# Kernel tuning notes

Hardware: AMD Instinct MI355X
Metric: run time of the kernel (lower is better)

The kernel has to match this reference:

```python
import jax, jax.numpy as jnp
import numpy as np
from jax import lax

SCALES = [0.5, 1, 2]


def resize_bilinear_ac(x, oh, ow):
    """F.interpolate(mode='bilinear', align_corners=True) for NCHW x."""
    B, C, H, W = x.shape
    def coords(n_in, n_out):
        c = jnp.linspace(0.0, n_in - 1.0, n_out).astype(x.dtype)
        i0 = jnp.clip(jnp.floor(c).astype(jnp.int32), 0, n_in - 1)
        i1 = jnp.minimum(i0 + 1, n_in - 1)
        return i0, i1, c - i0.astype(x.dtype)
    y0, y1, wy = coords(H, oh)
    x0, x1, wx = coords(W, ow)
    top = x[:, :, y0, :] * (1 - wy)[:, None] + x[:, :, y1, :] * wy[:, None]
    return top[:, :, :, x0] * (1 - wx) + top[:, :, :, x1] * wx


def interpolate4d(t, oh, ow):
    """Geometry.interpolate4d: bilinear resize of both spatial pairs of [b,h1,w1,h2,w2]."""
    b, h1, w1, h2, w2 = t.shape
    t = t.reshape(b, h1, w1, h2 * w2).transpose(0, 3, 1, 2)
    t = resize_bilinear_ac(t, oh, ow)            # [b, h2*w2, oh, ow]
    t = t.reshape(b, h2, w2, oh * ow).transpose(0, 3, 1, 2)
    t = resize_bilinear_ac(t, oh, ow)            # [b, oh*ow, oh, ow]
    return t.reshape(b, oh, ow, oh, ow)


def conv2d_same(x, w):
    return lax.conv_general_dilated(x, w, (1, 1), [(1, 1), (1, 1)],
                                    dimension_numbers=('NCHW', 'OIHW', 'NCHW'))


def conv3d_same(x, w, p):
    return lax.conv_general_dilated(x, w, (1, 1, 1), [(p, p)] * 3,
                                    dimension_numbers=('NCDHW', 'OIDHW', 'NCDHW'))


def fast4d(corr, kernel, bias=None):
    """4D conv (stride 1, same zero-padding) via per-slice 3D convs, mirroring chm.fast4d.
    corr: [b, ci, sh, sw, th, tw]; kernel: [co, ci, k, k, k, k]."""
    b, ci, sh, sw, th, tw = corr.shape
    co, k = kernel.shape[0], kernel.shape[2]
    p = k // 2
    x = corr.transpose(0, 2, 1, 3, 4, 5).reshape(b * sh, ci, sw, th, tw)
    out = jnp.zeros((b, co, sh, sw, th, tw), corr.dtype)
    for pidx in range(k):
        ic = conv3d_same(x, kernel[:, :, pidx], p)
        ic = ic.reshape(b, sh, co, sw, th, tw).transpose(0, 2, 1, 3, 4, 5)
        a0, a1 = max(p - pidx, 0), min(sh, sh + p - pidx)
        s0, s1 = max(pidx - p, 0), min(sh, sh + pidx - p)
        out = out.at[:, :, a0:a1].add(ic[:, :, s0:s1])
    if bias is not None:
        out = out + bias.reshape(1, co, 1, 1, 1, 1)
    return out


def chm6d(corr, kernel):
    """6D conv with kernel (K,K,kk,kk,kk,kk), same zero-padding, no bias (chm.fast6d).
    corr: [b, 1, S, S, h, w, h, w]; kernel: [1, 1, K, K, kk, kk, kk, kk]."""
    b, _, S, _, h, w, _, _ = corr.shape
    K, kk = kernel.shape[2], kernel.shape[4]
    pk = K // 2
    x = corr.transpose(0, 2, 3, 1, 4, 5, 6, 7).reshape(b * S * S, 1, h, w, h, w)
    ker = kernel.reshape(1, K * K, kk, kk, kk, kk).swapaxes(0, 1)  # [K*K, 1, kk...]
    y = fast4d(x, ker).reshape(b, S, S, K * K, h, w, h, w)
    yp = jnp.pad(y, ((0, 0), (pk, pk), (pk, pk), (0, 0), (0, 0), (0, 0), (0, 0), (0, 0)))
    out = jnp.zeros((b, S, S, h, w, h, w), corr.dtype)
    for ki in range(K):
        for kj in range(K):
            out = out + yp[:, ki:ki + S, kj:kj + S, ki * K + kj]
    return out[:, None]


def mutual_nn_filter(cm):
    smax = jnp.max(cm, axis=2, keepdims=True)
    tmax = jnp.max(cm, axis=1, keepdims=True)
    smax = jnp.where(smax == 0, 1e-30, smax)
    tmax = jnp.where(tmax == 0, 1e-30, tmax)
    return cm * ((cm / smax) * (cm / tmax))


def build_correlation6d(src_feat, trg_feat, conv_ws):
    bsz, _, side, _ = src_feat.shape
    sfs, tfs = [], []
    for scale, w in zip(SCALES, conv_ws):
        s = int(np.floor(scale * side))
        sfs.append(conv2d_same(resize_bilinear_ac(src_feat, s, s), w))
        tfs.append(conv2d_same(resize_bilinear_ac(trg_feat, s, s), w))
    corr6d = []
    for sf in sfs:
        ch, ss = sf.shape[1], sf.shape[-1]
        sv = sf.reshape(bsz, ch, ss * ss).transpose(0, 2, 1)   # [b, ss^2, ch]
        sn = jnp.linalg.norm(sv, axis=2, keepdims=True)
        for tf in tfs:
            ts = tf.shape[-1]
            tv = tf.reshape(bsz, ch, ts * ts)                  # [b, ch, ts^2]
            tn = jnp.linalg.norm(tv, axis=1, keepdims=True)
            c = jnp.einsum('bsc,bct->bst', sv, tv) / (sn * tn)
            corr6d.append(interpolate4d(c.reshape(bsz, ss, ss, ts, ts), side, side))
    corr = jnp.stack(corr6d).reshape(3, 3, bsz, side, side, side, side)
    corr = corr.transpose(2, 0, 1, 3, 4, 5, 6)                 # [b, 3, 3, s, s, s, s]
    return jnp.maximum(corr, 0.0)


def chm_forward(src_feat, trg_feat, w0, w1, w2, k6, k4, b4):
    bsz, _, side, _ = src_feat.shape
    corr = build_correlation6d(src_feat, trg_feat, (w0, w1, w2))[:, None]
    corr = jax.nn.sigmoid(chm6d(corr, k6))                     # [b,1,3,3,h,w,h,w]
    h = w = side
    corr = corr.reshape(bsz, -1, h, w, h, w).max(axis=1)       # max over 9 scale pairs
    corr = interpolate4d(corr, 2 * h, 2 * w)[:, None]          # [b,1,2h,2w,2h,2w]
    corr = jax.nn.softplus(fast4d(corr, k4, b4)[:, 0])
    n = corr.shape[-1] ** 2
    return mutual_nn_filter(corr.reshape(bsz, n, n))


def setup_inputs() -> dict:
    key = jax.random.key(0)
    ks = jax.random.split(key, 8)
    b, fd, side = 4, 1024, 16
    w_std = 0.02  # ~kaiming for 3x3 conv with fan_in 1024*9
    return {
        'src_feat': jax.random.normal(ks[0], (b, fd, side, side), jnp.float32),
        'trg_feat': jax.random.normal(ks[1], (b, fd, side, side), jnp.float32),
        'conv_w0': jax.random.normal(ks[2], (fd // 4, fd, 3, 3), jnp.float32) * w_std,
        'conv_w1': jax.random.normal(ks[3], (fd // 4, fd, 3, 3), jnp.float32) * w_std,
        'conv_w2': jax.random.normal(ks[4], (fd // 4, fd, 3, 3), jnp.float32) * w_std,
        'chm6d_w': jax.random.normal(ks[5], (1, 1, 3, 3, 5, 5, 5, 5), jnp.float32) * 0.05,
        'chm4d_w': jax.random.normal(ks[6], (1, 1, 5, 5, 5, 5), jnp.float32) * 0.05,
        'chm4d_b': jnp.zeros((1,), jnp.float32),
    }


def reference(src_feat, trg_feat, conv_w0, conv_w1, conv_w2, chm6d_w, chm4d_w, chm4d_b):
    return chm_forward(src_feat, trg_feat, conv_w0, conv_w1, conv_w2, chm6d_w, chm4d_w, chm4d_b)
```

## Files before the change

### kernel.cpp

```cpp
#include <hip/hip_runtime.h>
#include <cstdint>
#include <cstddef>


#define DEVFN __device__ __forceinline__

typedef __attribute__((ext_vector_type(8))) short short8v;
typedef __attribute__((ext_vector_type(4))) float f32x4;
typedef unsigned int u32;

DEVFN void gl_lds16(const void* g, void* l){
  __builtin_amdgcn_global_load_lds(
      (const __attribute__((address_space(1))) u32*)g,
      (__attribute__((address_space(3))) u32*)l, 16, 0, 0);
}

constexpr size_t OFF_WB    = 0;
constexpr size_t OFF_P8    = 3538944;
constexpr size_t OFF_P16   = 3948544;
constexpr size_t OFF_P32   = 5275648;
constexpr size_t OFF_SF8   = 10010624;
constexpr size_t OFF_TF8   = 10076160;
constexpr size_t OFF_SF16  = 10141696;
constexpr size_t OFF_TF16  = 10403840;
constexpr size_t OFF_SF32  = 10665984;
constexpr size_t OFF_TF32  = 11714560;
constexpr size_t OFF_INVS  = 12763136;
constexpr size_t OFF_INVT  = 12768512;
constexpr size_t OFF_TMAX  = 12777984;
constexpr size_t OFF_CORR6 = 12782080;
constexpr size_t OFF_CMAXP = OFF_CORR6 + 2359296 + 128;
constexpr size_t OFF_WA    = OFF_CMAXP + 131072;
constexpr size_t OFF_PARTK = OFF_WA + 96128;
constexpr size_t OFF_SMAXP = OFF_PARTK + 2752512;
constexpr size_t OFF_WA4   = OFF_SMAXP + 16384;
constexpr size_t OFF_FB3   = OFF_WA4 + 12800;
constexpr size_t WS_FLOATS = OFF_FB3 + 1376256;

__device__ constexpr size_t PAIR_OFF[9] = {
  OFF_WB + 0,       OFF_WB + 16384,   OFF_WB + 81920,
  OFF_WB + 344064,  OFF_WB + 409600,  OFF_WB + 671744,
  OFF_WB + 1720320, OFF_WB + 1982464, OFF_WB + 3031040 };
constexpr size_t OFF_CL    = 0;
constexpr size_t OFF_MAXED = 9437184;
constexpr size_t OFF_INT32 = 262144;

__device__ constexpr int SSARR[3] = {8, 16, 32};
__device__ constexpr int PAIR_START[9] = {0,4,20,84,100,164,420,484,740};

DEVFN unsigned short f2bf(float f){
  unsigned int u = __float_as_uint(f);
  return (unsigned short)((u + 0x7fffu + ((u >> 16) & 1u)) >> 16);
}
DEVFN float bf2f(unsigned short u){
  return __uint_as_float(((unsigned int)u) << 16);
}

__global__ __launch_bounds__(256) void k_wpack(const float* __restrict__ w0,
                                               const float* __restrict__ w1,
                                               const float* __restrict__ w2,
                                               float* __restrict__ wsf){
  int bx = blockIdx.x;
  int scale = bx >> 8, cg = (bx >> 4) & 15, ig = bx & 15;
  const float* w = (scale==0) ? w0 : (scale==1 ? w1 : w2);
  const int t = threadIdx.x;
  __shared__ float sW[16*580];
  const float* src = w + (size_t)cg*16*9216 + (size_t)ig*576;
  for (int i=t; i<9216; i+=256){
    int co = i/576, r = i%576;
    sW[co*580 + r] = src[(size_t)co*9216 + r];
  }
  __syncthreads();
  unsigned short* ob = (unsigned short*)(wsf + OFF_WB) + (size_t)scale*2359296;
  for (int f=t; f<1152; f+=256){
    int tap = f/128, rem = f%128, kcl = rem>>6, l = rem&63;
    int kc = ig*2 + kcl;
    int co = l & 15;
    int ciL = kcl*32 + ((l>>4)&3)*8;
    unsigned short* o = ob + ((size_t)tap*32768 + (size_t)kc*1024 + (size_t)cg*64 + l)*8;
    #pragma unroll
    for (int i=0;i<8;i++)
      o[i] = f2bf(sW[co*580 + (ciL+i)*9 + tap]);
  }
}

__global__ void k_wa(const float* __restrict__ k6, float* __restrict__ wsf){
  int gid = blockIdx.x*256 + threadIdx.x;
  if (gid >= 24000) return;
  int tap = gid / 192, rem = gid % 192;
  int kc = rem / 64, l = rem % 64;
  int d = tap % 5, ac = tap / 5, a = ac / 5, c = ac % 5;
  int so = l & 15, k8 = (l >> 4) * 8;
  unsigned short* o = (unsigned short*)(wsf + OFF_WA) + (size_t)gid*8;
  #pragma unroll
  for (int i=0;i<8;i++){
    int kg = kc*32 + k8 + i;
    int e = kg >> 4, pr = kg & 15;
    float v = 0.f;
    if (so < 9 && pr < 9 && e < 5){
      int pi = pr/3, pj = pr%3, sio = so/3, sjo = so%3;
      int ki = pi - sio + 1, kj = pj - sjo + 1;
      if (ki>=0 && ki<=2 && kj>=0 && kj<=2)
        v = k6[(((((ki*3+kj)*5 + a)*5 + c)*5 + d)*5) + e];
    }
    o[i] = f2bf(v);
  }
}

__global__ void k_wa4(const float* __restrict__ k4, float* __restrict__ wsf){
  int gid = blockIdx.x*256 + threadIdx.x;
  if (gid >= 3200) return;
  int d = gid / 640, rem = gid % 640;
  int kc = rem / 64, l = rem % 64;
  int so = l & 15, soy = so >> 2, sox = so & 3;
  int e = kc >> 1;
  int pyw = 4*(kc & 1) + (l >> 4);
  unsigned short* o = (unsigned short*)(wsf + OFF_WA4) + (size_t)gid*8;
  #pragma unroll
  for (int i=0;i<8;i++){
    int a = pyw - soy, c = i - sox;
    float v = 0.f;
    if (a>=0 && a<=4 && c>=0 && c<=4)
      v = k4[((a*5 + c)*5 + d)*5 + e];
    o[i] = f2bf(v);
  }
}

__global__ __launch_bounds__(256) void k_inpack(const float* __restrict__ src,
                                                const float* __restrict__ trg,
                                                float* __restrict__ wsf){
  int bt = blockIdx.x >> 6, cg = blockIdx.x & 63;
  int chbase = cg*16;
  int t = threadIdx.x;
  __shared__ float sIn[16][257];
  const float* gin = ((bt>=4)? trg : src) + ((size_t)(bt&3)*1024 + chbase)*256;
  #pragma unroll
  for (int i=0;i<16;i++){
    int idx = t + i*256; int ch = idx>>8, pos = idx&255;
    sIn[ch][pos] = gin[(size_t)ch*256 + pos];
  }
  __syncthreads();
  int ch = t & 15, pw = t >> 4;
  #pragma unroll 1
  for (int s=0; s<3; s++){
    int S = SSARR[s], Sp = S+2, Sp2 = Sp*Sp;
    size_t poff = (s==0)?OFF_P8 : (s==1)?OFF_P16 : OFF_P32;
    unsigned short* o = (unsigned short*)(wsf + poff) + (size_t)bt*Sp2*1024 + chbase + ch;
    float rs = 15.f/(float)(S-1);
    for (int i = pw; i < Sp2; i += 16){
      int py = i / Sp, px = i % Sp;
      float v = 0.f;
      if (py>0 && py<Sp-1 && px>0 && px<Sp-1){
        float cy = (float)(py-1)*rs, cx = (float)(px-1)*rs;
        int y0 = (int)cy; if (y0>15) y0=15; int y1 = (y0+1<16)?y0+1:15; float fy = cy-(float)y0;
        int x0 = (int)cx; if (x0>15) x0=15; int x1 = (x0+1<16)?x0+1:15; float fx = cx-(float)x0;
        v = (1.f-fy)*((1.f-fx)*sIn[ch][y0*16+x0] + fx*sIn[ch][y0*16+x1])
          +       fy*((1.f-fx)*sIn[ch][y1*16+x0] + fx*sIn[ch][y1*16+x1]);
      }
      o[(size_t)i*1024] = f2bf(v);
    }
  }
}

__global__ __launch_bounds__(256) void k_conv_mfma(float* __restrict__ wsf){
  int bxid = blockIdx.x;
  int scale, bt, cot, post, ks, S, lgS;
  if (bxid < 512){
    int xcd = bxid & 7, j2 = bxid >> 3;
    int g = (j2 >> 5)*8 + xcd;
    int j = j2 & 31;
    scale = 2; S = 32; lgS = 5;
    bt = g >> 1; cot = g & 1; post = j >> 1; ks = j & 1;
  } else {
    int r = bxid - 512;
    ks = r & 1; int bx = 256 + (r >> 1);
    if (bx < 320){ int q=bx-256; scale=1; S=16; lgS=4; bt=q>>3; cot=(q>>2)&1; post=q&3; }
    else         { int q=bx-320; scale=0; S=8;  lgS=3; bt=q>>1; cot=q&1; post=0; }
  }
  const int Sp = S+2, N = S*S;
  const unsigned short* WbS = (const unsigned short*)(wsf + OFF_WB) + (size_t)scale*2359296;
  size_t poff = scale==0?OFF_P8: scale==1?OFF_P16:OFF_P32;
  const unsigned short* Pb = (const unsigned short*)(wsf + poff) + (size_t)bt*Sp*Sp*1024;
  size_t obase = (scale==2) ? (bt>=4?OFF_TF32:OFF_SF32)
               : (scale==1) ? (bt>=4?OFF_TF16:OFF_SF16)
                            : (bt>=4?OFF_TF8 :OFF_SF8);
  if (ks) obase += OFF_PARTK - OFF_SF8;
  float* outp = wsf + obase + (size_t)(bt&3)*256*N;

  const int t = threadIdx.x, l = t&63, w = t>>6, wm = w&1, wn = w>>1;
  const int nc_base = cot*8;
  const int pos0 = post*64;
  const int it0 = ks*72, it1 = it0 + 72;

  __shared__ __align__(16) unsigned short Ab[2][8192];
  __shared__ __align__(16) unsigned short Bb[2][4096];

  f32x4 acc[4][2];
  #pragma unroll
  for (int i=0;i<4;i++)
    #pragma unroll
    for (int j=0;j<2;j++) acc[i][j] = (f32x4){0.f,0.f,0.f,0.f};

  auto STAGE = [&](int buf, int it){
    int tap = it>>4, kq = it&15;
    int dy = tap/3, dx = tap - dy*3;
    #pragma unroll
    for (int j=0;j<4;++j){
      int c = w + j*4;
      int kc = c>>3, nc = c&7;
      const unsigned short* src =
        WbS + ((((size_t)tap*32 + kq*2 + kc)*16 + nc_base + nc)*64 + l)*8;
      gl_lds16(src, &Ab[buf][c*512]);
    }
    #pragma unroll
    for (int j=0;j<2;++j){
      int c = w + j*4;
      int kc = c>>2, np = c&3;
      int pos = pos0 + np*16 + (l&15);
      int y = pos>>lgS, x = pos&(S-1);
      int row = (y+dy)*Sp + (x+dx);
      int ci = kq*64 + kc*32 + ((l>>4)<<3);
      gl_lds16(Pb + (size_t)row*1024 + ci, &Bb[buf][c*512]);
    }
  };

  STAGE(0, it0);
  __syncthreads();
  int buf = 0;
  #pragma unroll 1
  for (int it=it0; it<it1; ++it){
    if (it+1 < it1) STAGE(buf^1, it+1);
    #pragma unroll
    for (int kc=0; kc<2; ++kc){
      short8v a0 = *(const short8v*)&Ab[buf][((kc*8 + wm*4 + 0)*64 + l)*8];
      short8v a1 = *(const short8v*)&Ab[buf][((kc*8 + wm*4 + 1)*64 + l)*8];
      short8v a2 = *(const short8v*)&Ab[buf][((kc*8 + wm*4 + 2)*64 + l)*8];
      short8v a3 = *(const short8v*)&Ab[buf][((kc*8 + wm*4 + 3)*64 + l)*8];
      short8v b0 = *(const short8v*)&Bb[buf][((kc*4 + wn*2 + 0)*64 + l)*8];
      short8v b1 = *(const short8v*)&Bb[buf][((kc*4 + wn*2 + 1)*64 + l)*8];
      acc[0][0] = __builtin_amdgcn_mfma_f32_16x16x32_bf16(a0, b0, acc[0][0], 0,0,0);
      acc[1][0] = __builtin_amdgcn_mfma_f32_16x16x32_bf16(a1, b0, acc[1][0], 0,0,0);
      acc[2][0] = __builtin_amdgcn_mfma_f32_16x16x32_bf16(a2, b0, acc[2][0], 0,0,0);
      acc[3][0] = __builtin_amdgcn_mfma_f32_16x16x32_bf16(a3, b0, acc[3][0], 0,0,0);
      acc[0][1] = __builtin_amdgcn_mfma_f32_16x16x32_bf16(a0, b1, acc[0][1], 0,0,0);
      acc[1][1] = __builtin_amdgcn_mfma_f32_16x16x32_bf16(a1, b1, acc[1][1], 0,0,0);
      acc[2][1] = __builtin_amdgcn_mfma_f32_16x16x32_bf16(a2, b1, acc[2][1], 0,0,0);
      acc[3][1] = __builtin_amdgcn_mfma_f32_16x16x32_bf16(a3, b1, acc[3][1], 0,0,0);
    }
    __syncthreads();
    buf ^= 1;
  }

  const int r0 = (l>>4)*4, cl = l&15;
  float* ob = outp + (size_t)(cot*128 + wm*64)*N + pos0 + wn*32 + cl;
  #pragma unroll
  for (int mf=0; mf<4; ++mf)
    #pragma unroll
    for (int nf=0; nf<2; ++nf){
      float* op = ob + (size_t)(mf*16 + r0)*N + nf*16;
      #pragma unroll
      for (int i=0;i<4;++i) op[(size_t)i*N] = acc[mf][nf][i];
    }
}

__global__ __launch_bounds__(256) void k_fbpack(float* __restrict__ ws){
  int bx = blockIdx.x;
  int tsr = bx/84, r = bx%84;
  int s, b, chunk;
  if (r < 4)       { s=0; b=r;        chunk=0; }
  else if (r < 20) { s=1; int q=r-4;  b=q>>2; chunk=q&3; }
  else             { s=2; int q=r-20; b=q>>4; chunk=q&15; }
  int P = SSARR[s]*SSARR[s];
  size_t fbase = (s==0)? (tsr?OFF_TF8 :OFF_SF8)
               : (s==1)? (tsr?OFF_TF16:OFF_SF16)
                       : (tsr?OFF_TF32:OFF_SF32);
  const float* src = ws + fbase + (size_t)b*256*P;
  const float* prt = ws + OFF_PARTK + (fbase - OFF_SF8) + (size_t)b*256*P;
  int pos0 = chunk*64;
  const int t = threadIdx.x;
  __shared__ float tile[64][260];
  for (int i=0;i<64;i++){
    int idx = t + i*256; int ch = idx>>6, pl = idx&63;
    size_t o = (size_t)ch*P + pos0 + pl;
    tile[pl][ch] = src[o] + prt[o];
  }
  __syncthreads();
  int rowbase = tsr*5376 + (s==0?0: s==1?256:1280) + b*P + pos0;
  unsigned short* FB = (unsigned short*)(ws + OFF_FB3);
  for (int i=0;i<64;i++){
    int idx = t + i*256; int pl = idx>>8, ch = idx&255;
    FB[(size_t)(rowbase+pl)*256 + ch] = f2bf(tile[pl][ch]);
  }
}

__global__ void k_invnorm(float* __restrict__ ws){
  int gid = blockIdx.x*256 + threadIdx.x;
  int row = gid >> 4, sub = gid & 15;
  const unsigned short* fb = (const unsigned short*)(ws + OFF_FB3)
                           + (size_t)row*256 + sub*16;
  float s = 0.f;
  #pragma unroll
  for (int i=0;i<2;i++){
    short8v v = *(const short8v*)(fb + i*8);
    #pragma unroll
    for (int j=0;j<8;j++){
      float f = bf2f(((unsigned short*)&v)[j]);
      s = fmaf(f, f, s);
    }
  }
  #pragma unroll
  for (int m=1; m<16; m<<=1) s += __shfl_xor(s, m);
  if (sub == 0){
    int tsr = row/5376, r = row%5376;
    ws[(tsr ? OFF_INVT : OFF_INVS) + r] = 1.f/sqrtf(s);
  }
}

__global__ __launch_bounds__(256) void k_corr(float* __restrict__ ws){
  int bx = blockIdx.x;
  int p = (bx>=4)+(bx>=20)+(bx>=84)+(bx>=100)+(bx>=164)+(bx>=420)+(bx>=484)+(bx>=740);
  int si = p/3, ti = p%3;
  int M = SSARR[si]*SSARR[si], N = SSARR[ti]*SSARR[ti];
  int ntN = N >> 6;
  int rem = bx - PAIR_START[p];
  int b = rem & 3; rem >>= 2;
  int nt = rem % ntN, mt = rem / ntN;
  int m0 = mt*64, n0 = nt*64;
  const unsigned short* FB = (const unsigned short*)(ws + OFF_FB3);
  const unsigned short* Ap = FB + (size_t)((si==0?0: si==1?256:1280) + b*M + m0)*256;
  const unsigned short* Bp = FB + (size_t)(5376 + (ti==0?0: ti==1?256:1280) + b*N + n0)*256;
  const int t = threadIdx.x, l = t&63, w = t>>6, wm = w&1, wn = w>>1;
  const int mrow = wm*32 + (l&15), ncol = wn*32 + (l&15);
  f32x4 acc[2][2];
  #pragma unroll
  for (int i=0;i<2;i++)
    #pragma unroll
    for (int j=0;j<2;j++) acc[i][j] = (f32x4){0.f,0.f,0.f,0.f};
  #pragma unroll
  for (int ksp=0; ksp<8; ++ksp){
    const int ko = ksp*32 + ((l>>4)&3)*8;
    short8v a0 = *(const short8v*)(Ap + (size_t) mrow     *256 + ko);
    short8v a1 = *(const short8v*)(Ap + (size_t)(mrow+16) *256 + ko);
    short8v b0 = *(const short8v*)(Bp + (size_t) ncol     *256 + ko);
    short8v b1 = *(const short8v*)(Bp + (size_t)(ncol+16) *256 + ko);
    acc[0][0] = __builtin_amdgcn_mfma_f32_16x16x32_bf16(a0, b0, acc[0][0], 0,0,0);
    acc[1][0] = __builtin_amdgcn_mfma_f32_16x16x32_bf16(a1, b0, acc[1][0], 0,0,0);
    acc[0][1] = __builtin_amdgcn_mfma_f32_16x16x32_bf16(a0, b1, acc[0][1], 0,0,0);
    acc[1][1] = __builtin_amdgcn_mfma_f32_16x16x32_bf16(a1, b1, acc[1][1], 0,0,0);
  }
  const float* iS = ws + OFF_INVS + (si==0?0: si==1?256:1280) + (size_t)b*M;
  const float* iT = ws + OFF_INVT + (ti==0?0: ti==1?256:1280) + (size_t)b*N;
  float* C = ws + PAIR_OFF[p] + (size_t)b*M*N;
  const int r0 = (l>>4)*4, cl = l&15;
  #pragma unroll
  for (int mf=0; mf<2; ++mf)
    #pragma unroll
    for (int nf=0; nf<2; ++nf)
      #pragma unroll
      for (int i=0;i<4;++i){
        int m = m0 + wm*32 + mf*16 + r0 + i;
        int n = n0 + wn*32 + nf*16 + cl;
        C[(size_t)m*N + n] = acc[mf][nf][i]*iS[m]*iT[n];
      }
}

DEVFN void cw_coord(int i, int n, int OH, int& i0, int& i1, float& f){
  float c = (float)(i*(n-1))/(float)(OH-1);
  int a = (int)c; if (a > n-1) a = n-1;
  i0 = a; i1 = (a+1 < n) ? a+1 : n-1; f = c - (float)a;
}

__global__ __launch_bounds__(256) void k_interp_pairs(float* __restrict__ ws){
  int bx = blockIdx.x;
  int p = bx >> 10;
  int bl = bx & 1023;
  int b = bl >> 8, oy = (bl >> 4) & 15, ox = bl & 15;
  int si = p/3, ti = p%3;
  int h1 = SSARR[si], t1 = SSARR[ti], t12 = t1*t1;
  int y0,y1,x0,x1; float fy,fx;
  cw_coord(oy,h1,16,y0,y1,fy); cw_coord(ox,h1,16,x0,x1,fx);
  const float* in = ws + PAIR_OFF[p] + (size_t)b*h1*h1*t12;
  __shared__ float sPl[4][1024];
  const int t = threadIdx.x;
  {
    const float* pl0 = in + (size_t)(y0*h1+x0)*t12;
    const float* pl1 = in + (size_t)(y0*h1+x1)*t12;
    const float* pl2 = in + (size_t)(y1*h1+x0)*t12;
    const float* pl3 = in + (size_t)(y1*h1+x1)*t12;
    for (int i=t; i<t12; i+=256){
      sPl[0][i] = pl0[i]; sPl[1][i] = pl1[i];
      sPl[2][i] = pl2[i]; sPl[3][i] = pl3[i];
    }
  }
  __syncthreads();
  int px = t & 15, py = t >> 4;
  int u0,u1,v0,v1; float fu,fv;
  cw_coord(py,t1,16,u0,u1,fu); cw_coord(px,t1,16,v0,v1,fv);
  float wY[2]={1.f-fy,fy}, wX[2]={1.f-fx,fx};
  float wU[2]={1.f-fu,fu}, wV[2]={1.f-fv,fv};
  int us[2]={u0,u1}, vs[2]={v0,v1};
  float s = 0.f;
  #pragma unroll
  for (int qa=0; qa<2; qa++)
    #pragma unroll
    for (int qc=0; qc<2; qc++){
      float wyx = wY[qa]*wX[qc];
      const float* base = sPl[qa*2+qc];
      #pragma unroll
      for (int qu=0; qu<2; qu++)
        #pragma unroll
        for (int qv=0; qv<2; qv++)
          s += wyx*wU[qu]*wV[qv]*base[us[qu]*t1 + vs[qv]];
    }
  ws[OFF_CORR6 + ((size_t)b*9 + p)*65536 + ((size_t)(oy*16+ox)<<8) + t] = fmaxf(s, 0.f);
}

__global__ __launch_bounds__(256) void k_cl(float* __restrict__ ws){
  int bx = blockIdx.x;
  int b = bx >> 8, yx = bx & 255;
  const int t = threadIdx.x;
  __shared__ __align__(16) unsigned short tile[10080];
  for (int i=t; i<1260; i+=256)
    *reinterpret_cast<f32x4*>((float*)&tile[i*8]) = (f32x4){0.f,0.f,0.f,0.f};
  __syncthreads();
  const float* c6 = ws + OFF_CORR6 + ((size_t)b*9 << 16) + ((size_t)yx << 8);
  const int qy = t >> 4, qx = t & 15;
  const int wo = ((2+qy)*21 + 2+qx)*24;
  #pragma unroll
  for (int pr=0; pr<9; ++pr)
    tile[wo + pr] = f2bf(c6[((size_t)pr << 16) + t]);
  __syncthreads();
  unsigned short* o = (unsigned short*)(ws + OFF_CL) + (size_t)bx*10080;
  for (int i=t; i<1260; i+=256)
    *reinterpret_cast<f32x4*>((float*)&o[i*8]) =
      *reinterpret_cast<const f32x4*>((const float*)&tile[i*8]);
}

__global__ __launch_bounds__(256) void k_chm6d(float* __restrict__ ws){
  int id = (blockIdx.x & 7)*128 + (blockIdx.x >> 3);
  const int b = id >> 8, sy = (id >> 4) & 15, sx = id & 15;
  const int t = threadIdx.x, l = t & 63, w = t >> 6;
  const int x = l & 15, h = (l >> 4) & 1, e2 = (l >> 4) >> 1;
  const unsigned short* CLu = (const unsigned short*)(ws + OFF_CL);
  const unsigned short* WAu = (const unsigned short*)(ws + OFF_WA);
  __shared__ __align__(16) unsigned short tile[2][10080];

  f32x4 acc[4];
  #pragma unroll
  for (int i=0;i<4;i++) acc[i] = (f32x4){0.f,0.f,0.f,0.f};

  auto STAGE = [&](int buf, int YX){
    const unsigned short* src = CLu + (size_t)(b*256 + YX)*10080;
    #pragma unroll
    for (int j=0;j<5;++j){
      int ch = t + j*256;
      if (ch < 1260) gl_lds16(src + (size_t)ch*8, &tile[buf][ch*8]);
    }
  };

  const int xb0 = (x + e2)*24 + 8*h;

  int i0 = 0;
  for (; i0 < 25; ++i0){
    int Y = sy + i0/5 - 2, X = sx + i0%5 - 2;
    if (Y>=0 && Y<=15 && X>=0 && X<=15) break;
  }
  {
    int Y = sy + i0/5 - 2, X = sx + i0%5 - 2;
    STAGE(0, Y*16 + X);
  }
  __syncthreads();
  int buf = 0, i = i0;
  #pragma unroll 1
  while (i < 25){
    int nx = i + 1;
    for (; nx < 25; ++nx){
      int Y = sy + nx/5 - 2, X = sx + nx%5 - 2;
      if (Y>=0 && Y<=15 && X>=0 && X<=15) break;
    }
    if (nx < 25){
      int Y = sy + nx/5 - 2, X = sx + nx%5 - 2;
      STAGE(buf^1, Y*16 + X);
    }
    {
      const unsigned short* wa = WAu + (size_t)i*5*3*512;
      short8v afr[5][3];
      #pragma unroll
      for (int d=0; d<5; ++d)
        #pragma unroll
        for (int kc=0; kc<3; ++kc)
          afr[d][kc] = *(const short8v*)&wa[((d*3 + kc)*64 + l)*8];
      const unsigned short* tb = &tile[buf][0];
      #pragma unroll
      for (int rl=0; rl<8; ++rl){
        const int row = (w*4 + rl)*504;
        short8v bf0 = *(const short8v*)&tb[row + xb0];
        short8v bf1 = *(const short8v*)&tb[row + xb0 + 48];
        short8v bf2 = *(const short8v*)&tb[row + xb0 + 96];
        #pragma unroll
        for (int y=0; y<4; ++y){
          if (y <= rl && rl - y <= 4){
            const int d = rl - y;
            acc[y] = __builtin_amdgcn_mfma_f32_16x16x32_bf16(afr[d][0], bf0, acc[y], 0,0,0);
            acc[y] = __builtin_amdgcn_mfma_f32_16x16x32_bf16(afr[d][1], bf1, acc[y], 0,0,0);
            acc[y] = __builtin_amdgcn_mfma_f32_16x16x32_bf16(afr[d][2], bf2, acc[y], 0,0,0);
          }
        }
      }
    }
    __syncthreads();
    buf ^= 1; i = nx;
  }

  const int g = l >> 4;
  float* maxed = ws + OFF_MAXED + (size_t)b*65536 + (size_t)(sy*16+sx)*256;
  #pragma unroll
  for (int y=0; y<4; ++y){
    float lm;
    if (g < 2)      lm = fmaxf(fmaxf(acc[y][0], acc[y][1]), fmaxf(acc[y][2], acc[y][3]));
    else if (g==2)  lm = acc[y][0];
    else            lm = -1e30f;
    lm = fmaxf(lm, __shfl_xor(lm, 16));
    lm = fmaxf(lm, __shfl_xor(lm, 32));
    if (l < 16)
      maxed[(w*4 + y)*16 + x] = 1.f/(1.f + expf(-lm));
  }
}

__global__ void k_interp32(float* __restrict__ ws){
  int id = blockIdx.x*256 + threadIdx.x;
  int px = id & 31, py = (id>>5)&31, ox = (id>>10)&31, oy = (id>>15)&31, b = id>>20;
  int y0,y1,x0,x1,u0,u1,v0,v1; float fy,fx,fu,fv;
  cw_coord(oy,16,32,y0,y1,fy); cw_coord(ox,16,32,x0,x1,fx);
  cw_coord(py,16,32,u0,u1,fu); cw_coord(px,16,32,v0,v1,fv);
  const float* in = ws + OFF_MAXED + (size_t)b*65536;
  int ys[2]={y0,y1}, xs[2]={x0,x1}, us[2]={u0,u1}, vs[2]={v0,v1};
  float wy[2]={1.f-fy,fy}, wx[2]={1.f-fx,fx}, wu[2]={1.f-fu,fu}, wv[2]={1.f-fv,fv};
  float s = 0.f;
  #pragma unroll
  for (int ia=0; ia<2; ia++)
    #pragma unroll
    for (int ic=0; ic<2; ic++){
      float wyx = wy[ia]*wx[ic];
      const float* base = in + ((size_t)ys[ia]*16 + xs[ic])*256;
      #pragma unroll
      for (int id_=0; id_<2; id_++)
        #pragma unroll
        for (int ie=0; ie<2; ie++)
          s += wyx*wu[id_]*wv[ie]*base[(size_t)us[id_]*16 + vs[ie]];
    }
  ws[OFF_INT32 + id] = s;
}

__global__ __launch_bounds__(256) void k_fast4d(float* __restrict__ ws,
                                                const float* __restrict__ b4,
                                                float* __restrict__ out){
  int id = (blockIdx.x & 7)*128 + (blockIdx.x >> 3);
  const int b = id >> 8, rem = id & 255;
  const int syb = rem >> 5, sxb = (rem >> 2) & 7, yh = rem & 3;
  const int t = threadIdx.x, l = t & 63, w = t >> 6;
  __shared__ __align__(16) unsigned short T[27648];
  __shared__ float red[4][16];
  for (int i=t; i<3456; i+=256)
    *reinterpret_cast<f32x4*>((float*)&T[i*8]) = (f32x4){0.f,0.f,0.f,0.f};
  __syncthreads();
  const float* I = ws + OFF_INT32 + (size_t)b*1048576;
  #pragma unroll 4
  for (int j=0; j<48; ++j){
    int idx2 = j*256 + t;
    int xo = idx2 & 15, pl = (idx2>>4) & 63, ry = idx2 >> 10;
    int pya = syb*4 + (pl>>3) - 2;
    int pxa = sxb*4 + (pl&7) - 2;
    int rya = yh*8 + ry - 2;
    if (pya>=0 && pya<32 && pxa>=0 && pxa<32 && rya>=0 && rya<32){
      float2 v = *reinterpret_cast<const float2*>(
          I + (size_t)(pya*32+pxa)*1024 + rya*32 + xo*2);
      int base = (ry*36 + xo*2 + 2)*64 + pl;
      T[base]      = f2bf(v.x);
      T[base + 64] = f2bf(v.y);
    }
  }
  __syncthreads();
  const unsigned short* WA4 = (const unsigned short*)(ws + OFF_WA4);
  f32x4 acc[2][2];
  #pragma unroll
  for (int i=0;i<2;i++)
    #pragma unroll
    for (int j=0;j<2;j++) acc[i][j] = (f32x4){0.f,0.f,0.f,0.f};
  const unsigned short* Tl = T + (l&15)*64 + (l>>4)*8 + w*2*2304;
  #pragma unroll 1
  for (int d=0; d<5; ++d){
    short8v afr[10];
    #pragma unroll
    for (int kc=0; kc<10; ++kc)
      afr[kc] = *(const short8v*)&WA4[((size_t)(d*10 + kc)*64 + l)*8];
    #pragma unroll
    for (int y2=0; y2<2; ++y2){
      const unsigned short* Tr = Tl + (y2 + d)*2304;
      #pragma unroll
      for (int xg=0; xg<2; ++xg){
        const unsigned short* Tx = Tr + xg*1024;
        #pragma unroll
        for (int kc=0; kc<10; ++kc){
          short8v bf = *(const short8v*)&Tx[(kc>>1)*64 + (kc&1)*32];
          acc[y2][xg] = __builtin_amdgcn_mfma_f32_16x16x32_bf16(afr[kc], bf, acc[y2][xg], 0,0,0);
        }
      }
    }
  }
  const float bias = b4[0];
  float rm[4] = {-1e30f,-1e30f,-1e30f,-1e30f};
  #pragma unroll
  for (int y2=0; y2<2; ++y2)
    #pragma unroll
    for (int xg=0; xg<2; ++xg)
      #pragma unroll
      for (int i=0; i<4; ++i){
        int so = (l>>4)*4 + i;
        float xv = acc[y2][xg][i] + bias;
        float sp = fmaxf(xv,0.f) + log1pf(expf(-fabsf(xv)));
        int row = (syb*4 + (so>>2))*32 + sxb*4 + (so&3);
        int col = (yh*8 + w*2 + y2)*32 + xg*16 + (l&15);
        out[((size_t)b*1024 + row)*1024 + col] = sp;
        rm[i] = fmaxf(rm[i], sp);
      }
  #pragma unroll
  for (int m=1; m<16; m<<=1)
    #pragma unroll
    for (int i=0;i<4;++i) rm[i] = fmaxf(rm[i], __shfl_xor(rm[i], m));
  if ((l & 15) == 0){
    #pragma unroll
    for (int i=0;i<4;++i) red[w][(l>>4)*4 + i] = rm[i];
  }
  __syncthreads();
  if (t < 16){
    float m = fmaxf(fmaxf(red[0][t], red[1][t]), fmaxf(red[2][t], red[3][t]));
    int row = (syb*4 + (t>>2))*32 + sxb*4 + (t&3);
    ws[OFF_SMAXP + (size_t)yh*4096 + (size_t)b*1024 + row] = m;
  }
}

__global__ void k_colmax_p(const float* __restrict__ cm, float* __restrict__ ws){
  int b = blockIdx.x >> 7, rg = (blockIdx.x >> 2) & 31, cg = blockIdx.x & 3;
  int c = cg*256 + threadIdx.x;
  const float* base = cm + (size_t)b*1048576 + (size_t)rg*32768 + c;
  float m = -1e30f;
  #pragma unroll 4
  for (int r=0; r<32; r++) m = fmaxf(m, base[(size_t)r*1024]);
  ws[OFF_CMAXP + (size_t)(b*32+rg)*1024 + c] = m;
}

__global__ void k_colmax_r(float* __restrict__ ws){
  int id = blockIdx.x*256 + threadIdx.x;
  int b = id >> 10, c = id & 1023;
  float m = -1e30f;
  #pragma unroll
  for (int rg=0; rg<32; rg++)
    m = fmaxf(m, ws[OFF_CMAXP + (size_t)(b*32+rg)*1024 + c]);
  ws[OFF_TMAX + id] = m;
}

__global__ void k_mutual(float* __restrict__ cm, const float* __restrict__ ws){
  int id = blockIdx.x*256 + threadIdx.x;
  int b = id >> 20, r = (id>>10)&1023, c = id&1023;
  float v  = cm[id];
  size_t si = (size_t)(b<<10) + r;
  float sm = fmaxf(fmaxf(ws[OFF_SMAXP + si],        ws[OFF_SMAXP + 4096 + si]),
                   fmaxf(ws[OFF_SMAXP + 8192 + si], ws[OFF_SMAXP + 12288 + si]));
  float tm = ws[OFF_TMAX + (b<<10) + c];
  sm = (sm==0.f) ? 1e-30f : sm;
  tm = (tm==0.f) ? 1e-30f : tm;
  cm[id] = v * (v/sm) * (v/tm);
}

extern "C" void kernel_launch(void* const* d_in, const int* in_sizes, int n_in,
                              void* d_out, int out_size, void* d_ws, size_t ws_size,
                              hipStream_t stream){
  const float* src = (const float*)d_in[0];
  const float* trg = (const float*)d_in[1];
  const float* w0  = (const float*)d_in[2];
  const float* w1  = (const float*)d_in[3];
  const float* w2  = (const float*)d_in[4];
  const float* k6  = (const float*)d_in[5];
  const float* k4  = (const float*)d_in[6];
  const float* b4  = (const float*)d_in[7];
  float* ws  = (float*)d_ws;
  float* out = (float*)d_out;
  (void)in_sizes; (void)n_in; (void)out_size; (void)ws_size;

  k_wpack       <<<768,   256, 0, stream>>>(w0, w1, w2, ws);
  k_wa          <<<94,    256, 0, stream>>>(k6, ws);
  k_wa4         <<<13,    256, 0, stream>>>(k4, ws);
  k_inpack      <<<512,   256, 0, stream>>>(src, trg, ws);
  k_conv_mfma   <<<672,   256, 0, stream>>>(ws);
  k_fbpack      <<<168,   256, 0, stream>>>(ws);
  k_invnorm     <<<672,   256, 0, stream>>>(ws);
  k_corr        <<<1764,  256, 0, stream>>>(ws);
  k_interp_pairs<<<9216,  256, 0, stream>>>(ws);
  k_cl          <<<1024,  256, 0, stream>>>(ws);
  k_chm6d       <<<1024,  256, 0, stream>>>(ws);
  k_interp32    <<<16384, 256, 0, stream>>>(ws);
  k_fast4d      <<<1024,  256, 0, stream>>>(ws, b4, out);
  k_colmax_p    <<<512,   256, 0, stream>>>(out, ws);
  k_colmax_r    <<<16,    256, 0, stream>>>(ws);
  k_mutual      <<<16384, 256, 0, stream>>>(out, ws);
}
```

Before: 371.1 us.

## Widen conv MFMA tile to 128 positions and remap blocks across XCDs

The bf16 MFMA conv kernel is templated on the number of N-fragments, so scales 16 and 32 use a 128-position tile (4 N-fragments per wave) and scale 8 keeps 64. Each staged weight tile is therefore reused over twice as many positions, which halves weight reloads. The grid shrinks from 672 to 352 blocks and uses an XCD-interleaved block index. The cost is more accumulator registers, a larger B buffer in LDS (64 KB total), and fewer blocks to fill the CUs.

```diff
diff --git a/kernel.cpp b/kernel.cpp
--- a/kernel.cpp
+++ b/kernel.cpp
@@ -162,20 +162,93 @@
   }
 }
 
+template<int NF>
+DEVFN void conv_core(const unsigned short* __restrict__ WbS,
+                     const unsigned short* __restrict__ Pb,
+                     float* __restrict__ outp,
+                     int S, int lgS, int Sp, int N,
+                     int nc_base, int pos0, int it0, int it1, int t,
+                     unsigned short (&Ab)[2][8192], unsigned short (&Bb)[2][8192]){
+  const int l = t&63, w = t>>6, wm = w&1, wn = w>>1;
+  f32x4 acc[4][NF];
+  #pragma unroll
+  for (int i=0;i<4;i++)
+    #pragma unroll
+    for (int j=0;j<NF;j++) acc[i][j] = (f32x4){0.f,0.f,0.f,0.f};
+
+  auto STAGE = [&](int buf, int it){
+    int tap = it>>4, kq = it&15;
+    int dy = tap/3, dx = tap - dy*3;
+    #pragma unroll
+    for (int j=0;j<4;++j){
+      int c = w + j*4;
+      int kc = c>>3, nc = c&7;
+      const unsigned short* src =
+        WbS + ((((size_t)tap*32 + kq*2 + kc)*16 + nc_base + nc)*64 + l)*8;
+      gl_lds16(src, &Ab[buf][c*512]);
+    }
+    #pragma unroll
+    for (int j=0;j<NF;++j){
+      int c = w + j*4;
+      int kc = (NF==4)? (c>>3) : (c>>2);
+      int np = (NF==4)? (c&7)  : (c&3);
+      int pos = pos0 + np*16 + (l&15);
+      int y = pos>>lgS, x = pos&(S-1);
+      int row = (y+dy)*Sp + (x+dx);
+      int ci = kq*64 + kc*32 + ((l>>4)<<3);
+      gl_lds16(Pb + (size_t)row*1024 + ci, &Bb[buf][c*512]);
+    }
+  };
+
+  STAGE(0, it0);
+  __syncthreads();
+  int buf = 0;
+  #pragma unroll 1
+  for (int it=it0; it<it1; ++it){
+    if (it+1 < it1) STAGE(buf^1, it+1);
+    #pragma unroll
+    for (int kc=0; kc<2; ++kc){
+      short8v a[4], bv[NF];
+      #pragma unroll
+      for (int mf=0; mf<4; ++mf)
+        a[mf] = *(const short8v*)&Ab[buf][((kc*8 + wm*4 + mf)*64 + l)*8];
+      #pragma unroll
+      for (int nf=0; nf<NF; ++nf)
+        bv[nf] = *(const short8v*)&Bb[buf][((kc*(2*NF) + wn*NF + nf)*64 + l)*8];
+      #pragma unroll
+      for (int mf=0; mf<4; ++mf)
+        #pragma unroll
+        for (int nf=0; nf<NF; ++nf)
+          acc[mf][nf] = __builtin_amdgcn_mfma_f32_16x16x32_bf16(a[mf], bv[nf], acc[mf][nf], 0,0,0);
+    }
+    __syncthreads();
+    buf ^= 1;
+  }
+
+  const int r0 = (l>>4)*4, cl = l&15;
+  float* ob = outp + (size_t)(wm*64)*N + pos0 + wn*(NF*16) + cl;
+  #pragma unroll
+  for (int mf=0; mf<4; ++mf)
+    #pragma unroll
+    for (int nf=0; nf<NF; ++nf){
+      float* op = ob + (size_t)(mf*16 + r0)*N + nf*16;
+      #pragma unroll
+      for (int i=0;i<4;++i) op[(size_t)i*N] = acc[mf][nf][i];
+    }
+}
+
 __global__ __launch_bounds__(256) void k_conv_mfma(float* __restrict__ wsf){
-  int bxid = blockIdx.x;
-  int scale, bt, cot, post, ks, S, lgS;
-  if (bxid < 512){
-    int xcd = bxid & 7, j2 = bxid >> 3;
-    int g = (j2 >> 5)*8 + xcd;
-    int j = j2 & 31;
-    scale = 2; S = 32; lgS = 5;
-    bt = g >> 1; cot = g & 1; post = j >> 1; ks = j & 1;
+  int bx = (blockIdx.x & 7)*44 + (blockIdx.x >> 3);
+  int scale, bt, cot, post, ks, nf, S, lgS;
+  if (bx < 256){
+    scale=2; S=32; lgS=5; nf=4;
+    bt = bx>>5; int r = bx&31; cot = r>>4; r &= 15; post = r>>1; ks = r&1;
+  } else if (bx < 320){
+    int q = bx-256; scale=1; S=16; lgS=4; nf=4;
+    bt = q>>3; cot = (q>>2)&1; post = (q>>1)&1; ks = q&1;
   } else {
-    int r = bxid - 512;
-    ks = r & 1; int bx = 256 + (r >> 1);
-    if (bx < 320){ int q=bx-256; scale=1; S=16; lgS=4; bt=q>>3; cot=(q>>2)&1; post=q&3; }
-    else         { int q=bx-320; scale=0; S=8;  lgS=3; bt=q>>1; cot=q&1; post=0; }
+    int q = bx-320; scale=0; S=8; lgS=3; nf=2;
+    bt = q>>2; cot = (q>>1)&1; ks = q&1; post = 0;
   }
   const int Sp = S+2, N = S*S;
   const unsigned short* WbS = (const unsigned short*)(wsf + OFF_WB) + (size_t)scale*2359296;
@@ -185,82 +258,20 @@
                : (scale==1) ? (bt>=4?OFF_TF16:OFF_SF16)
                             : (bt>=4?OFF_TF8 :OFF_SF8);
   if (ks) obase += OFF_PARTK - OFF_SF8;
-  float* outp = wsf + obase + (size_t)(bt&3)*256*N;
-
-  const int t = threadIdx.x, l = t&63, w = t>>6, wm = w&1, wn = w>>1;
+  float* outp = wsf + obase + (size_t)(bt&3)*256*N + (size_t)(cot*128)*N;
   const int nc_base = cot*8;
-  const int pos0 = post*64;
+  const int pos0 = post*(nf*32);
   const int it0 = ks*72, it1 = it0 + 72;
 
   __shared__ __align__(16) unsigned short Ab[2][8192];
-  __shared__ __align__(16) unsigned short Bb[2][4096];
-
-  f32x4 acc[4][2];
-  #pragma unroll
-  for (int i=0;i<4;i++)
-    #pragma unroll
-    for (int j=0;j<2;j++) acc[i][j] = (f32x4){0.f,0.f,0.f,0.f};
-
-  auto STAGE = [&](int buf, int it){
-    int tap = it>>4, kq = it&15;
-    int dy = tap/3, dx = tap - dy*3;
-    #pragma unroll
-    for (int j=0;j<4;++j){
-      int c = w + j*4;
-      int kc = c>>3, nc = c&7;
-      const unsigned short* src =
-        WbS + ((((size_t)tap*32 + kq*2 + kc)*16 + nc_base + nc)*64 + l)*8;
-      gl_lds16(src, &Ab[buf][c*512]);
-    }
-    #pragma unroll
-    for (int j=0;j<2;++j){
-      int c = w + j*4;
-      int kc = c>>2, np = c&3;
-      int pos = pos0 + np*16 + (l&15);
-      int y = pos>>lgS, x = pos&(S-1);
-      int row = (y+dy)*Sp + (x+dx);
-      int ci = kq*64 + kc*32 + ((l>>4)<<3);
-      gl_lds16(Pb + (size_t)row*1024 + ci, &Bb[buf][c*512]);
-    }
-  };
-
-  STAGE(0, it0);
-  __syncthreads();
-  int buf = 0;
-  #pragma unroll 1
-  for (int it=it0; it<it1; ++it){
-    if (it+1 < it1) STAGE(buf^1, it+1);
-    #pragma unroll
-    for (int kc=0; kc<2; ++kc){
-      short8v a0 = *(const short8v*)&Ab[buf][((kc*8 + wm*4 + 0)*64 + l)*8];
-      short8v a1 = *(const short8v*)&Ab[buf][((kc*8 + wm*4 + 1)*64 + l)*8];
-      short8v a2 = *(const short8v*)&Ab[buf][((kc*8 + wm*4 + 2)*64 + l)*8];
-      short8v a3 = *(const short8v*)&Ab[buf][((kc*8 + wm*4 + 3)*64 + l)*8];
-      short8v b0 = *(const short8v*)&Bb[buf][((kc*4 + wn*2 + 0)*64 + l)*8];
-      short8v b1 = *(const short8v*)&Bb[buf][((kc*4 + wn*2 + 1)*64 + l)*8];
-      acc[0][0] = __builtin_amdgcn_mfma_f32_16x16x32_bf16(a0, b0, acc[0][0], 0,0,0);
-      acc[1][0] = __builtin_amdgcn_mfma_f32_16x16x32_bf16(a1, b0, acc[1][0], 0,0,0);
-      acc[2][0] = __builtin_amdgcn_mfma_f32_16x16x32_bf16(a2, b0, acc[2][0], 0,0,0);
-      acc[3][0] = __builtin_amdgcn_mfma_f32_16x16x32_bf16(a3, b0, acc[3][0], 0,0,0);
-      acc[0][1] = __builtin_amdgcn_mfma_f32_16x16x32_bf16(a0, b1, acc[0][1], 0,0,0);
-      acc[1][1] = __builtin_amdgcn_mfma_f32_16x16x32_bf16(a1, b1, acc[1][1], 0,0,0);
-      acc[2][1] = __builtin_amdgcn_mfma_f32_16x16x32_bf16(a2, b1, acc[2][1], 0,0,0);
-      acc[3][1] = __builtin_amdgcn_mfma_f32_16x16x32_bf16(a3, b1, acc[3][1], 0,0,0);
-    }
-    __syncthreads();
-    buf ^= 1;
-  }
-
-  const int r0 = (l>>4)*4, cl = l&15;
-  float* ob = outp + (size_t)(cot*128 + wm*64)*N + pos0 + wn*32 + cl;
-  #pragma unroll
-  for (int mf=0; mf<4; ++mf)
-    #pragma unroll
-    for (int nf=0; nf<2; ++nf){
-      float* op = ob + (size_t)(mf*16 + r0)*N + nf*16;
-      #pragma unroll
-      for (int i=0;i<4;++i) op[(size_t)i*N] = acc[mf][nf][i];
-    }
+  __shared__ __align__(16) unsigned short Bb[2][8192];
+
+  if (nf==4)
+    conv_core<4>(WbS, Pb, outp, S, lgS, Sp, N, nc_base, pos0, it0, it1,
+                 threadIdx.x, Ab, Bb);
+  else
+    conv_core<2>(WbS, Pb, outp, S, lgS, Sp, N, nc_base, pos0, it0, it1,
+                 threadIdx.x, Ab, Bb);
 }
 
 __global__ __launch_bounds__(256) void k_fbpack(float* __restrict__ ws){
@@ -692,7 +703,7 @@
   k_wa          <<<94,    256, 0, stream>>>(k6, ws);
   k_wa4         <<<13,    256, 0, stream>>>(k4, ws);
   k_inpack      <<<512,   256, 0, stream>>>(src, trg, ws);
-  k_conv_mfma   <<<672,   256, 0, stream>>>(ws);
+  k_conv_mfma   <<<352,   256, 0, stream>>>(ws);
   k_fbpack      <<<168,   256, 0, stream>>>(ws);
   k_invnorm     <<<672,   256, 0, stream>>>(ws);
   k_corr        <<<1764,  256, 0, stream>>>(ws);
```

After: 386.4 us. +4.1%, slower.
